# Kernel tuning notes

Hardware: AMD Instinct MI355X
Metric: run time of the kernel (lower is better)

## Reference

```python
import jax, jax.numpy as jnp
import numpy as np

N, CIN, COUT, K, S, H, W = 16, 512, 512, 3, 512, 64, 64
EPS = 1e-8


def setup_inputs() -> dict:
    key = jax.random.key(0)
    k1, k2, k3, k4 = jax.random.split(key, 4)
    return {
        "x": jax.random.normal(k1, (N, CIN, H, W), jnp.float32),
        "style": jax.random.normal(k2, (N, S), jnp.float32),
        # conv weight ~ N(0,1) as in the torch module (lr_mul=1)
        "weight": jax.random.normal(k3, (COUT, CIN, K, K), jnp.float32),
        # style modulation linear: weight ~ N(0,1), bias init 1.0
        "style_w": jax.random.normal(k4, (CIN, S), jnp.float32),
        "style_b": jnp.ones((CIN,), jnp.float32),
    }


def reference(x, style, weight, style_w, style_b):
    # equalized-lr scales (gain=1.0, lr_mul=1.0, mode=fan_in)
    lin_scale = 1.0 / jnp.sqrt(jnp.float32(S))          # fan_in of linear = style_channels
    w_scale = 1.0 / jnp.sqrt(jnp.float32(CIN * K * K))  # fan_in of weight[0] = Cin*k*k

    # style modulation: s[n, cin] (style_bias = 0.0)
    s = style @ (style_w.T * lin_scale) + style_b        # [N, Cin]

    w = weight * w_scale                                  # [Cout, Cin, K, K]

    # demodulation: rsqrt(sum_{i,kh,kw} (w[o,i]*s[n,i])^2 + eps) per (n, o)
    demod = jax.lax.rsqrt(jnp.einsum('oikl,ni->no', w * w, s * s) + EPS)  # [N, Cout]

    # fused form: conv(x * s, W) * demod  ==  grouped conv with per-sample modulated weights
    xs = x * s[:, :, None, None]
    out = jax.lax.conv_general_dilated(
        xs, w, window_strides=(1, 1), padding='SAME',
        dimension_numbers=('NCHW', 'OIHW', 'NCHW'))
    return out * demod[:, :, None, None]
```

## Files before the change

### kernel.cpp

```cpp
#include <hip/hip_runtime.h>
#include <hip/hip_bf16.h>

#define CIN   512
#define COUT  512
#define HW    4096
#define PADW  66
#define NB    16
#define KTOT  4608
#define BUFSZ 65536
#define BOFF  32768

static constexpr float LIN_SCALE = 0.044194173824159216f;
static constexpr float W_SCALE   = 0.014731391274719738f;

typedef __attribute__((ext_vector_type(8))) short bf16x8;
typedef __attribute__((ext_vector_type(4))) float f32x4;

__device__ __forceinline__ unsigned short f2us(float f) {
    __hip_bfloat16 h = __float2bfloat16(f); unsigned short u; __builtin_memcpy(&u, &h, 2); return u;
}

typedef const __attribute__((address_space(1))) unsigned int guint;
typedef __attribute__((address_space(3))) unsigned int luint;
__device__ __forceinline__ void gload_lds16(const void* g, void* l) {
    __builtin_amdgcn_global_load_lds((guint*)g, (luint*)l, 16, 0, 0);
}

__global__ void k_style(const float* __restrict__ style,
                        const float* __restrict__ style_w,
                        const float* __restrict__ style_b,
                        float* __restrict__ s) {
    int wid  = (blockIdx.x * blockDim.x + threadIdx.x) >> 6;
    int lane = threadIdx.x & 63;
    int n = wid >> 9, i = wid & 511;
    float sum = 0.f;
    for (int j = lane; j < 512; j += 64)
        sum += style[n * 512 + j] * style_w[i * 512 + j];
    for (int m = 32; m; m >>= 1) sum += __shfl_xor(sum, m, 64);
    if (lane == 0) s[n * 512 + i] = sum * LIN_SCALE + style_b[i];
}

__global__ void k_wprep(const float* __restrict__ weight,
                        float* __restrict__ wsq,
                        __hip_bfloat16* __restrict__ wt) {
    int oi = blockIdx.x * 256 + threadIdx.x;
    int o = oi >> 9, i = oi & 511;
    float sq = 0.f;
#pragma unroll
    for (int tp = 0; tp < 9; ++tp) {
        float v = weight[(size_t)oi * 9 + tp] * W_SCALE;
        sq += v * v;
        wt[(size_t)o * KTOT + tp * 512 + i] = __float2bfloat16(v);
    }
    wsq[oi] = sq;
}

__global__ void k_demod(const float* __restrict__ wsq, const float* __restrict__ s,
                        float* __restrict__ demod) {
    int wid  = (blockIdx.x * blockDim.x + threadIdx.x) >> 6;
    int lane = threadIdx.x & 63;
    int n = wid >> 9, o = wid & 511;
    float sum = 0.f;
    for (int i = lane; i < 512; i += 64) {
        float sv = s[n * 512 + i];
        sum += wsq[o * 512 + i] * sv * sv;
    }
    for (int m = 32; m; m >>= 1) sum += __shfl_xor(sum, m, 64);
    if (lane == 0) demod[n * 512 + o] = rsqrtf(sum + 1e-8f);
}

__global__ void k_xs(const float* __restrict__ x, const float* __restrict__ s,
                     __hip_bfloat16* __restrict__ xs) {
    const int n = blockIdx.y;
    const int t = threadIdx.x;
    if (blockIdx.x == 64) {
        uint4 z = make_uint4(0u, 0u, 0u, 0u);
        for (int idx = t; idx < 16640; idx += 256) {
            int bp = idx >> 6, sl = idx & 63;
            int hp, wp;
            if (bp < 66)       { hp = 0;  wp = bp; }
            else if (bp < 132) { hp = 65; wp = bp - 66; }
            else { int k2 = bp - 132; hp = 1 + (k2 >> 1); wp = (k2 & 1) ? 65 : 0; }
            *(uint4*)(xs + (((size_t)n * PADW * PADW) + hp * PADW + wp) * 512 + sl * 8) = z;
        }
        return;
    }
    const int h = blockIdx.x;
    const int PITCH = 65;
    __shared__ float lds[64 * 65];
    __shared__ float sv[512];
    sv[t] = s[n * 512 + t];
    sv[t + 256] = s[n * 512 + 256 + t];
    for (int ic = 0; ic < 8; ++ic) {
        const int i0 = ic * 64;
        __syncthreads();
#pragma unroll
        for (int j = 0; j < 4; ++j) {
            int idx = j * 256 + t;
            int il = idx >> 4;
            int wq = (idx & 15) * 4;
            float4 v = *(const float4*)(x + (((size_t)n * 512 + i0 + il) * HW) + h * 64 + wq);
            float* dst = &lds[il * PITCH + wq];
            dst[0] = v.x; dst[1] = v.y; dst[2] = v.z; dst[3] = v.w;
        }
        __syncthreads();
#pragma unroll
        for (int j = 0; j < 2; ++j) {
            int idx = j * 256 + t;
            int wp = idx >> 3;
            int ib = (idx & 7) * 8;
            unsigned short tmp[8];
#pragma unroll
            for (int r = 0; r < 8; ++r) {
                float xv = lds[(ib + r) * PITCH + wp];
                tmp[r] = f2us(xv * sv[i0 + ib + r]);
            }
            uint4 o;
            o.x = (unsigned)tmp[0] | ((unsigned)tmp[1] << 16);
            o.y = (unsigned)tmp[2] | ((unsigned)tmp[3] << 16);
            o.z = (unsigned)tmp[4] | ((unsigned)tmp[5] << 16);
            o.w = (unsigned)tmp[6] | ((unsigned)tmp[7] << 16);
            *(uint4*)(xs + ((size_t)((n * PADW + h + 1) * PADW + (wp + 1))) * 512 + i0 + ib) = o;
        }
    }
}

#define BAR __builtin_amdgcn_s_barrier()
#define SB0 __builtin_amdgcn_sched_barrier(0)
#define LD_B(dst, CH) { _Pragma("unroll") for (int t_ = 0; t_ < 4; ++t_) \
    dst[t_] = *(const bf16x8*)(cb + BOFF + bRow + t_ * 2048 + (CH)); }
#define LD_A(dst, MG, CH) { _Pragma("unroll") for (int t_ = 0; t_ < 4; ++t_) \
    dst[t_] = *(const bf16x8*)(cb + aRow + ((MG) * 4 + t_) * 2048 + (CH)); }
#define MFMA_G(MG, AF, BF) { __builtin_amdgcn_s_setprio(1); \
    _Pragma("unroll") for (int m_ = 0; m_ < 4; ++m_) \
    _Pragma("unroll") for (int n_ = 0; n_ < 4; ++n_) \
        acc[(MG) * 4 + m_][n_] = __builtin_amdgcn_mfma_f32_16x16x32_bf16( \
            AF[m_], BF[n_], acc[(MG) * 4 + m_][n_], 0, 0, 0); \
    __builtin_amdgcn_s_setprio(0); }

__global__ __launch_bounds__(512, 2) void k_conv(
        const __hip_bfloat16* __restrict__ wt,
        const __hip_bfloat16* __restrict__ xs,
        const float* __restrict__ demod,
        float* __restrict__ out) {
    __shared__ __attribute__((aligned(16))) char smem[2 * BUFSZ];
    const int tid  = threadIdx.x;
    const int wv   = tid >> 6, lane = tid & 63;
    const int wm   = wv >> 2,  wn   = wv & 3;

    const int bid = blockIdx.x;
    const int xcd = bid & 7, idx = bid >> 3;
    const int pT  = idx & 15;
    const int o0  = ((idx >> 4) & 1) * 256;
    const int smp = xcd * 2 + (idx >> 5);

    const __hip_bfloat16* xsn = xs + (size_t)smp * (PADW * PADW * 512);

    const int rw = lane >> 3, cl = lane & 7;
    const int lc = cl ^ rw;
    const size_t aOff = (size_t)(wv * 8 + rw) * KTOT + lc * 8;
    const size_t bOff = (size_t)(wv * 8 + rw) * 512  + lc * 8;
    const __hip_bfloat16* aStage = wt  + (size_t)o0 * KTOT + aOff;
    const __hip_bfloat16* bStage = xsn + bOff;

    const int col = lane & 15, qd = lane >> 4;
    const int ch0 = ((qd)     ^ (col & 7)) << 4;
    const int ch1 = ((qd + 4) ^ (col & 7)) << 4;
    const int aRow = (wm * 128 + col) * 128;
    const int bRow = (wn * 64  + col) * 128;

    f32x4 acc[8][4] = {};

    {
        char* nbB = smem + BOFF + wv * 1024;
        char* nbA = smem + wv * 1024;
        const __hip_bfloat16* bS = bStage + (size_t)(pT * 4) * 33792;
        gload_lds16(bS,              nbB);
        gload_lds16(bS + 33792,      nbB + 8192);
        gload_lds16(bS + 2 * 33792,  nbB + 2 * 8192);
        gload_lds16(bS + 3 * 33792,  nbB + 3 * 8192);
        gload_lds16(aStage,              nbA);
        gload_lds16(aStage + 294912,     nbA + 8192);
        gload_lds16(aStage + 2 * 294912, nbA + 2 * 8192);
        gload_lds16(aStage + 3 * 294912, nbA + 3 * 8192);
        asm volatile("s_waitcnt vmcnt(0)" ::: "memory");
        BAR;
    }

    for (int kt = 0; kt < 71; ++kt) {
        const char* cb = smem + (kt & 1) * BUFSZ;
        char* nb = smem + ((kt + 1) & 1) * BUFSZ;
        const int kt1  = kt + 1;
        const int tap1 = kt1 >> 3, c1 = kt1 & 7;
        const int kh1  = tap1 / 3, kw1 = tap1 - kh1 * 3;
        const __hip_bfloat16* aS = aStage + (size_t)kt1 * 64;
        const __hip_bfloat16* bS = bStage +
            (size_t)((pT * 4 + kh1) * PADW + kw1) * 512 + c1 * 64;
        char* nbB = nb + BOFF + wv * 1024;
        char* nbA = nb + wv * 1024;

        bf16x8 bf0[4], bf1[4], afA[4], afB[4];

        LD_B(bf0, ch0); LD_A(afA, 0, ch0); LD_A(afB, 1, ch0);
        gload_lds16(bS,             nbB);
        gload_lds16(bS + 33792,     nbB + 8192);
        gload_lds16(bS + 2 * 33792, nbB + 2 * 8192);
        gload_lds16(bS + 3 * 33792, nbB + 3 * 8192);
        BAR;
        asm volatile("s_waitcnt lgkmcnt(4)" ::: "memory"); SB0;
        MFMA_G(0, afA, bf0);
        BAR;

        LD_B(bf1, ch1); LD_A(afA, 0, ch1);
        gload_lds16(aS,              nbA);
        gload_lds16(aS + 294912,     nbA + 8192);
        gload_lds16(aS + 2 * 294912, nbA + 2 * 8192);
        gload_lds16(aS + 3 * 294912, nbA + 3 * 8192);
        BAR;
        asm volatile("s_waitcnt lgkmcnt(8)" ::: "memory"); SB0;
        MFMA_G(1, afB, bf0);
        BAR;

        LD_A(afB, 1, ch1);
        BAR;
        asm volatile("s_waitcnt lgkmcnt(4)" ::: "memory"); SB0;
        MFMA_G(0, afA, bf1);
        BAR;

        asm volatile("s_waitcnt lgkmcnt(0)" ::: "memory"); SB0;
        MFMA_G(1, afB, bf1);
        asm volatile("s_waitcnt vmcnt(0)" ::: "memory");
        BAR;
    }

    {
        const char* cb = smem + BUFSZ;
        bf16x8 bf0[4], bf1[4], afA[4], afB[4];
        LD_B(bf0, ch0); LD_A(afA, 0, ch0); MFMA_G(0, afA, bf0);
        LD_A(afB, 1, ch0);                 MFMA_G(1, afB, bf0);
        LD_B(bf1, ch1); LD_A(afA, 0, ch1); MFMA_G(0, afA, bf1);
        LD_A(afB, 1, ch1);                 MFMA_G(1, afB, bf1);
    }

    const int hwBase = pT * 256 + wn * 64 + col;
#pragma unroll
    for (int m = 0; m < 8; ++m) {
#pragma unroll
        for (int rg = 0; rg < 4; ++rg) {
            const int o = o0 + wm * 128 + m * 16 + qd * 4 + rg;
            const float dm = demod[smp * 512 + o];
            float* orow = out + ((size_t)(smp * COUT + o)) * HW + hwBase;
#pragma unroll
            for (int nn = 0; nn < 4; ++nn)
                orow[nn * 16] = acc[m][nn][rg] * dm;
        }
    }
}

extern "C" void kernel_launch(void* const* d_in, const int* in_sizes, int n_in,
                              void* d_out, int out_size, void* d_ws, size_t ws_size,
                              hipStream_t stream) {
    const float* x       = (const float*)d_in[0];
    const float* style   = (const float*)d_in[1];
    const float* weight  = (const float*)d_in[2];
    const float* style_w = (const float*)d_in[3];
    const float* style_b = (const float*)d_in[4];
    float* out = (float*)d_out;

    char* ws = (char*)d_ws;
    float*          s_buf  = (float*)(ws + 0);
    float*          wsq    = (float*)(ws + 32768);
    float*          demod  = (float*)(ws + 1081344);
    __hip_bfloat16* wt     = (__hip_bfloat16*)(ws + 1114112);
    __hip_bfloat16* xs     = (__hip_bfloat16*)(ws + 5832704);

    k_style <<<dim3(2048),     dim3(256), 0, stream>>>(style, style_w, style_b, s_buf);
    k_wprep <<<dim3(1024),     dim3(256), 0, stream>>>(weight, wsq, wt);
    k_demod <<<dim3(2048),     dim3(256), 0, stream>>>(wsq, s_buf, demod);
    k_xs    <<<dim3(65, 16),   dim3(256), 0, stream>>>(x, s_buf, xs);
    k_conv  <<<dim3(512),      dim3(512), 0, stream>>>(wt, xs, demod, out);
}
```

Baseline: 512.3 us.

## Merge prep kernels, widen xs blocks, and drop mid-loop barriers in conv

Merges the style and weight-prep kernels into one launch and makes the xs staging kernel process two rows per 512-thread block. In the conv main loop, all global-to-LDS prefetches are issued up front and the intermediate workgroup barriers are removed. The loop instead relies only on lgkmcnt waits between fragment loads and MFMA groups, with one B fragment buffer shared across groups. This cuts launch overhead and barrier stalls, at the cost of less explicit ordering between waves and different register pressure.

```diff
diff --git a/kernel.cpp b/kernel.cpp
--- a/kernel.cpp
+++ b/kernel.cpp
@@ -26,33 +26,35 @@
     __builtin_amdgcn_global_load_lds((guint*)g, (luint*)l, 16, 0, 0);
 }
 
-__global__ void k_style(const float* __restrict__ style,
-                        const float* __restrict__ style_w,
-                        const float* __restrict__ style_b,
-                        float* __restrict__ s) {
-    int wid  = (blockIdx.x * blockDim.x + threadIdx.x) >> 6;
-    int lane = threadIdx.x & 63;
-    int n = wid >> 9, i = wid & 511;
-    float sum = 0.f;
-    for (int j = lane; j < 512; j += 64)
-        sum += style[n * 512 + j] * style_w[i * 512 + j];
-    for (int m = 32; m; m >>= 1) sum += __shfl_xor(sum, m, 64);
-    if (lane == 0) s[n * 512 + i] = sum * LIN_SCALE + style_b[i];
-}
-
-__global__ void k_wprep(const float* __restrict__ weight,
-                        float* __restrict__ wsq,
-                        __hip_bfloat16* __restrict__ wt) {
-    int oi = blockIdx.x * 256 + threadIdx.x;
-    int o = oi >> 9, i = oi & 511;
-    float sq = 0.f;
-#pragma unroll
-    for (int tp = 0; tp < 9; ++tp) {
-        float v = weight[(size_t)oi * 9 + tp] * W_SCALE;
-        sq += v * v;
-        wt[(size_t)o * KTOT + tp * 512 + i] = __float2bfloat16(v);
-    }
-    wsq[oi] = sq;
+__global__ void k_prep(const float* __restrict__ weight,
+                       const float* __restrict__ style,
+                       const float* __restrict__ style_w,
+                       const float* __restrict__ style_b,
+                       float* __restrict__ wsq,
+                       __hip_bfloat16* __restrict__ wt,
+                       float* __restrict__ s) {
+    const int bid = blockIdx.x;
+    if (bid < 1024) {
+        int oi = bid * 256 + threadIdx.x;
+        int o = oi >> 9, i = oi & 511;
+        float sq = 0.f;
+#pragma unroll
+        for (int tp = 0; tp < 9; ++tp) {
+            float v = weight[(size_t)oi * 9 + tp] * W_SCALE;
+            sq += v * v;
+            wt[(size_t)o * KTOT + tp * 512 + i] = __float2bfloat16(v);
+        }
+        wsq[oi] = sq;
+    } else {
+        int wid  = (bid - 1024) * 4 + (threadIdx.x >> 6);
+        int lane = threadIdx.x & 63;
+        int n = wid >> 9, i = wid & 511;
+        float sum = 0.f;
+        for (int j = lane; j < 512; j += 64)
+            sum += style[n * 512 + j] * style_w[i * 512 + j];
+        for (int m = 32; m; m >>= 1) sum += __shfl_xor(sum, m, 64);
+        if (lane == 0) s[n * 512 + i] = sum * LIN_SCALE + style_b[i];
+    }
 }
 
 __global__ void k_demod(const float* __restrict__ wsq, const float* __restrict__ s,
@@ -73,9 +75,9 @@
                      __hip_bfloat16* __restrict__ xs) {
     const int n = blockIdx.y;
     const int t = threadIdx.x;
-    if (blockIdx.x == 64) {
+    if (blockIdx.x == 32) {
         uint4 z = make_uint4(0u, 0u, 0u, 0u);
-        for (int idx = t; idx < 16640; idx += 256) {
+        for (int idx = t; idx < 16640; idx += 512) {
             int bp = idx >> 6, sl = idx & 63;
             int hp, wp;
             if (bp < 66)       { hp = 0;  wp = bp; }
@@ -85,34 +87,36 @@
         }
         return;
     }
-    const int h = blockIdx.x;
+    const int half = t >> 8;
+    const int tt   = t & 255;
+    const int h    = blockIdx.x * 2 + half;
     const int PITCH = 65;
-    __shared__ float lds[64 * 65];
+    __shared__ float lds[2][64 * 65];
     __shared__ float sv[512];
+    float* ld = lds[half];
     sv[t] = s[n * 512 + t];
-    sv[t + 256] = s[n * 512 + 256 + t];
     for (int ic = 0; ic < 8; ++ic) {
         const int i0 = ic * 64;
         __syncthreads();
 #pragma unroll
         for (int j = 0; j < 4; ++j) {
-            int idx = j * 256 + t;
+            int idx = j * 256 + tt;
             int il = idx >> 4;
             int wq = (idx & 15) * 4;
             float4 v = *(const float4*)(x + (((size_t)n * 512 + i0 + il) * HW) + h * 64 + wq);
-            float* dst = &lds[il * PITCH + wq];
+            float* dst = &ld[il * PITCH + wq];
             dst[0] = v.x; dst[1] = v.y; dst[2] = v.z; dst[3] = v.w;
         }
         __syncthreads();
 #pragma unroll
         for (int j = 0; j < 2; ++j) {
-            int idx = j * 256 + t;
+            int idx = j * 256 + tt;
             int wp = idx >> 3;
             int ib = (idx & 7) * 8;
             unsigned short tmp[8];
 #pragma unroll
             for (int r = 0; r < 8; ++r) {
-                float xv = lds[(ib + r) * PITCH + wp];
+                float xv = ld[(ib + r) * PITCH + wp];
                 tmp[r] = f2us(xv * sv[i0 + ib + r]);
             }
             uint4 o;
@@ -127,15 +131,16 @@
 
 #define BAR __builtin_amdgcn_s_barrier()
 #define SB0 __builtin_amdgcn_sched_barrier(0)
-#define LD_B(dst, CH) { _Pragma("unroll") for (int t_ = 0; t_ < 4; ++t_) \
-    dst[t_] = *(const bf16x8*)(cb + BOFF + bRow + t_ * 2048 + (CH)); }
-#define LD_A(dst, MG, CH) { _Pragma("unroll") for (int t_ = 0; t_ < 4; ++t_) \
+#define LGKM(N) asm volatile("s_waitcnt lgkmcnt(" #N ")" ::: "memory")
+#define LOAD_BF(CH) { _Pragma("unroll") for (int t_ = 0; t_ < 4; ++t_) \
+    bfv[t_] = *(const bf16x8*)(cb + BOFF + bRow + t_ * 2048 + (CH)); }
+#define LOAD_AF(dst, MG, CH) { _Pragma("unroll") for (int t_ = 0; t_ < 4; ++t_) \
     dst[t_] = *(const bf16x8*)(cb + aRow + ((MG) * 4 + t_) * 2048 + (CH)); }
-#define MFMA_G(MG, AF, BF) { __builtin_amdgcn_s_setprio(1); \
+#define MFMA_Q(BASE, AF) { __builtin_amdgcn_s_setprio(1); \
     _Pragma("unroll") for (int m_ = 0; m_ < 4; ++m_) \
     _Pragma("unroll") for (int n_ = 0; n_ < 4; ++n_) \
-        acc[(MG) * 4 + m_][n_] = __builtin_amdgcn_mfma_f32_16x16x32_bf16( \
-            AF[m_], BF[n_], acc[(MG) * 4 + m_][n_], 0, 0, 0); \
+        acc[(BASE) + m_][n_] = __builtin_amdgcn_mfma_f32_16x16x32_bf16( \
+            AF[m_], bfv[n_], acc[(BASE) + m_][n_], 0, 0, 0); \
     __builtin_amdgcn_s_setprio(0); }
 
 __global__ __launch_bounds__(512, 2) void k_conv(
@@ -189,57 +194,57 @@
 
     for (int kt = 0; kt < 71; ++kt) {
         const char* cb = smem + (kt & 1) * BUFSZ;
-        char* nb = smem + ((kt + 1) & 1) * BUFSZ;
+        char* nb = (char*)smem + ((kt + 1) & 1) * BUFSZ;
         const int kt1  = kt + 1;
         const int tap1 = kt1 >> 3, c1 = kt1 & 7;
-        const int kh1  = tap1 / 3, kw1 = tap1 - kh1 * 3;
+        const int kh1  = (tap1 * 11) >> 5;
+        const int kw1  = tap1 - kh1 * 3;
         const __hip_bfloat16* aS = aStage + (size_t)kt1 * 64;
         const __hip_bfloat16* bS = bStage +
             (size_t)((pT * 4 + kh1) * PADW + kw1) * 512 + c1 * 64;
         char* nbB = nb + BOFF + wv * 1024;
         char* nbA = nb + wv * 1024;
 
-        bf16x8 bf0[4], bf1[4], afA[4], afB[4];
-
-        LD_B(bf0, ch0); LD_A(afA, 0, ch0); LD_A(afB, 1, ch0);
-        gload_lds16(bS,             nbB);
-        gload_lds16(bS + 33792,     nbB + 8192);
-        gload_lds16(bS + 2 * 33792, nbB + 2 * 8192);
-        gload_lds16(bS + 3 * 33792, nbB + 3 * 8192);
-        BAR;
-        asm volatile("s_waitcnt lgkmcnt(4)" ::: "memory"); SB0;
-        MFMA_G(0, afA, bf0);
-        BAR;
-
-        LD_B(bf1, ch1); LD_A(afA, 0, ch1);
+        gload_lds16(bS,              nbB);
+        gload_lds16(bS + 33792,      nbB + 8192);
+        gload_lds16(bS + 2 * 33792,  nbB + 2 * 8192);
+        gload_lds16(bS + 3 * 33792,  nbB + 3 * 8192);
         gload_lds16(aS,              nbA);
         gload_lds16(aS + 294912,     nbA + 8192);
         gload_lds16(aS + 2 * 294912, nbA + 2 * 8192);
         gload_lds16(aS + 3 * 294912, nbA + 3 * 8192);
-        BAR;
-        asm volatile("s_waitcnt lgkmcnt(8)" ::: "memory"); SB0;
-        MFMA_G(1, afB, bf0);
-        BAR;
-
-        LD_A(afB, 1, ch1);
-        BAR;
-        asm volatile("s_waitcnt lgkmcnt(4)" ::: "memory"); SB0;
-        MFMA_G(0, afA, bf1);
-        BAR;
-
-        asm volatile("s_waitcnt lgkmcnt(0)" ::: "memory"); SB0;
-        MFMA_G(1, afB, bf1);
+
+        bf16x8 bfv[4], afE[4], afO[4];
+
+        LOAD_BF(ch0);
+        LOAD_AF(afE, 0, ch0);
+        LOAD_AF(afO, 1, ch0);
+        LGKM(4); SB0;
+        MFMA_Q(0, afE);
+        LOAD_AF(afE, 0, ch1);
+        LGKM(4); SB0;
+        MFMA_Q(4, afO);
+        LOAD_BF(ch1);
+        LOAD_AF(afO, 1, ch1);
+        LGKM(4); SB0;
+        MFMA_Q(0, afE);
+        LGKM(0); SB0;
+        MFMA_Q(4, afO);
+
         asm volatile("s_waitcnt vmcnt(0)" ::: "memory");
         BAR;
     }
 
     {
         const char* cb = smem + BUFSZ;
-        bf16x8 bf0[4], bf1[4], afA[4], afB[4];
-        LD_B(bf0, ch0); LD_A(afA, 0, ch0); MFMA_G(0, afA, bf0);
-        LD_A(afB, 1, ch0);                 MFMA_G(1, afB, bf0);
-        LD_B(bf1, ch1); LD_A(afA, 0, ch1); MFMA_G(0, afA, bf1);
-        LD_A(afB, 1, ch1);                 MFMA_G(1, afB, bf1);
+        bf16x8 bfv[4], afE[4], afO[4];
+        LOAD_BF(ch0); LOAD_AF(afE, 0, ch0); LOAD_AF(afO, 1, ch0);
+        LGKM(4); SB0; MFMA_Q(0, afE);
+        LOAD_AF(afE, 0, ch1);
+        LGKM(4); SB0; MFMA_Q(4, afO);
+        LOAD_BF(ch1); LOAD_AF(afO, 1, ch1);
+        LGKM(4); SB0; MFMA_Q(0, afE);
+        LGKM(0); SB0; MFMA_Q(4, afO);
     }
 
     const int hwBase = pT * 256 + wn * 64 + col;
@@ -274,9 +279,9 @@
     __hip_bfloat16* wt     = (__hip_bfloat16*)(ws + 1114112);
     __hip_bfloat16* xs     = (__hip_bfloat16*)(ws + 5832704);
 
-    k_style <<<dim3(2048),     dim3(256), 0, stream>>>(style, style_w, style_b, s_buf);
-    k_wprep <<<dim3(1024),     dim3(256), 0, stream>>>(weight, wsq, wt);
-    k_demod <<<dim3(2048),     dim3(256), 0, stream>>>(wsq, s_buf, demod);
-    k_xs    <<<dim3(65, 16),   dim3(256), 0, stream>>>(x, s_buf, xs);
-    k_conv  <<<dim3(512),      dim3(512), 0, stream>>>(wt, xs, demod, out);
-}
+    k_prep  <<<dim3(3072),    dim3(256), 0, stream>>>(weight, style, style_w, style_b,
+                                                      wsq, wt, s_buf);
+    k_xs    <<<dim3(33, 16),  dim3(512), 0, stream>>>(x, s_buf, xs);
+    k_demod <<<dim3(2048),    dim3(256), 0, stream>>>(wsq, s_buf, demod);
+    k_conv  <<<dim3(512),     dim3(512), 0, stream>>>(wt, xs, demod, out);
+}
```

New measurement: 503.8 us. About the same (-1.7%).
